# Performance work log

Measured on AMD Instinct MI355X. Metric: run time of the kernel, lower is better.

## Reference

```python
import jax, jax.numpy as jnp
import numpy as np

N, E, F_IN, HID, HEADS, B, CLASSES = 50000, 800000, 128, 64, 4, 512, 2


def setup_inputs() -> dict:
    key = jax.random.key(0)
    ks = jax.random.split(key, 20)
    s = 0.05
    inp = {
        "x": jax.random.normal(ks[0], (N, F_IN), jnp.float32),
        "edge_index": jax.random.randint(ks[1], (2, E), 0, N, jnp.int32),
        "batch": jnp.sort(jax.random.randint(ks[2], (N,), 0, B, jnp.int32)),
        # GCN layers (3): layer0 F_IN->HID, layers 1,2 HID->HID
        "gcn_w0": jax.random.normal(ks[3], (F_IN, HID), jnp.float32) * s,
        "gcn_b0": jnp.zeros((HID,), jnp.float32),
        "gcn_w1": jax.random.normal(ks[4], (HID, HID), jnp.float32) * s,
        "gcn_b1": jnp.zeros((HID,), jnp.float32),
        "gcn_w2": jax.random.normal(ks[5], (HID, HID), jnp.float32) * s,
        "gcn_b2": jnp.zeros((HID,), jnp.float32),
        # GAT: W [HID, HEADS*HID], attention vectors [HEADS, HID], bias [HID] (concat=False)
        "gat_w": jax.random.normal(ks[6], (HID, HEADS * HID), jnp.float32) * s,
        "gat_att_src": jax.random.normal(ks[7], (HEADS, HID), jnp.float32) * s,
        "gat_att_dst": jax.random.normal(ks[8], (HEADS, HID), jnp.float32) * s,
        "gat_b": jnp.zeros((HID,), jnp.float32),
        # MLP head
        "lin1_w": jax.random.normal(ks[9], (HID, HID // 2), jnp.float32) * s,
        "lin1_b": jnp.zeros((HID // 2,), jnp.float32),
        "lin2_w": jax.random.normal(ks[10], (HID // 2, CLASSES), jnp.float32) * s,
        "lin2_b": jnp.zeros((CLASSES,), jnp.float32),
    }
    return inp


def _forward(x, edge_index, batch,
             gcn_w0, gcn_b0, gcn_w1, gcn_b1, gcn_w2, gcn_b2,
             gat_w, gat_att_src, gat_att_dst, gat_b,
             lin1_w, lin1_b, lin2_w, lin2_b):
    n = x.shape[0]
    loop = jnp.arange(n, dtype=edge_index.dtype)
    src = jnp.concatenate([edge_index[0], loop])  # [E+N] with self-loops
    dst = jnp.concatenate([edge_index[1], loop])

    # symmetric GCN normalization (self-loops included, deg >= 1)
    deg = jax.ops.segment_sum(jnp.ones_like(dst, dtype=x.dtype), dst, num_segments=n)
    dinv = jax.lax.rsqrt(jnp.maximum(deg, 1.0))
    norm = dinv[src] * dinv[dst]  # [E+N]

    for W, b in ((gcn_w0, gcn_b0), (gcn_w1, gcn_b1), (gcn_w2, gcn_b2)):
        h = x @ W  # [N, HID]
        x = jax.ops.segment_sum(h[src] * norm[:, None], dst, num_segments=n) + b
        x = jax.nn.relu(x)  # dropout is identity in eval mode

    # GAT layer (heads=HEADS, concat=False -> mean over heads)
    H, C = gat_att_src.shape
    h = (x @ gat_w).reshape(n, H, C)  # [N, H, C]
    a_src = jnp.einsum('nhc,hc->nh', h, gat_att_src)
    a_dst = jnp.einsum('nhc,hc->nh', h, gat_att_dst)
    e = jax.nn.leaky_relu(a_src[src] + a_dst[dst], 0.2)  # [E+N, H]
    m = jax.ops.segment_max(e, dst, num_segments=n)      # per-dst softmax max
    p = jnp.exp(e - m[dst])
    denom = jax.ops.segment_sum(p, dst, num_segments=n)
    alpha = p / denom[dst]                                # [E+N, H]
    out = jax.ops.segment_sum(h[src] * alpha[:, :, None], dst, num_segments=n)
    x = jax.nn.relu(out.mean(axis=1) + gat_b)             # [N, HID]

    # global mean pool + global max pool over graphs
    cnt = jax.ops.segment_sum(jnp.ones((n,), x.dtype), batch, num_segments=B)
    mean_p = jax.ops.segment_sum(x, batch, num_segments=B) / jnp.maximum(cnt, 1.0)[:, None]
    max_p = jax.ops.segment_max(x, batch, num_segments=B)
    max_p = jnp.where(cnt[:, None] > 0, max_p, 0.0)
    g = mean_p + max_p  # [B, HID]

    g = jax.nn.relu(g @ lin1_w + lin1_b)
    return g @ lin2_w + lin2_b  # [B, CLASSES]


def reference(x, edge_index, batch,
              gcn_w0, gcn_b0, gcn_w1, gcn_b1, gcn_w2, gcn_b2,
              gat_w, gat_att_src, gat_att_dst, gat_b,
              lin1_w, lin1_b, lin2_w, lin2_b):
    return _forward(x, edge_index, batch,
                    gcn_w0, gcn_b0, gcn_w1, gcn_b1, gcn_w2, gcn_b2,
                    gat_w, gat_att_src, gat_att_dst, gat_b,
                    lin1_w, lin1_b, lin2_w, lin2_b)
```

## Files before the change

### kernel.cpp

```cpp
#include <hip/hip_runtime.h>
#include <math.h>

typedef short bf8 __attribute__((ext_vector_type(8)));
typedef _Float16 h8 __attribute__((ext_vector_type(8)));
typedef float f4 __attribute__((ext_vector_type(4)));
typedef unsigned short ushort_t;

#define BRANGE 128
#define NB_E 256

__device__ __forceinline__ int ilanebcast(int v, int l) {
  return __builtin_amdgcn_readlane(v, l);
}

__device__ __forceinline__ float wave_sum(float v) {
#pragma unroll
  for (int off = 32; off > 0; off >>= 1) v += __shfl_xor(v, off, 64);
  return v;
}

__device__ __forceinline__ ushort_t f2bf(float x) {
  unsigned int u = __float_as_uint(x);
  return (ushort_t)((u + 0x7fffu + ((u >> 16) & 1u)) >> 16);
}
__device__ __forceinline__ float b2f(ushort_t h) {
  return __uint_as_float(((unsigned int)h) << 16);
}

__global__ __launch_bounds__(256) void k_ehist(const int* __restrict__ dst,
                                               int* __restrict__ bhistT, int E, int nbuk) {
  __shared__ int h[512];
  int b = blockIdx.x, tid = threadIdx.x;
  for (int i = tid; i < nbuk; i += 256) h[i] = 0;
  __syncthreads();
  int chunk = (E + gridDim.x - 1) / gridDim.x;
  int e0 = b * chunk, e1 = min(E, e0 + chunk);
  for (int e = e0 + tid; e < e1; e += 256) atomicAdd(&h[dst[e] >> 7], 1);
  __syncthreads();
  for (int i = tid; i < nbuk; i += 256) bhistT[i * NB_E + b] = h[i];
}

__global__ __launch_bounds__(256) void k_btot(const int* __restrict__ bhistT,
                                              int* __restrict__ bcnt, int nb) {
  __shared__ int sm[256];
  int b = blockIdx.x, tid = threadIdx.x;
  sm[tid] = (tid < nb) ? bhistT[b * NB_E + tid] : 0;
  __syncthreads();
  for (int off = 128; off > 0; off >>= 1) {
    if (tid < off) sm[tid] += sm[tid + off];
    __syncthreads();
  }
  if (tid == 0) bcnt[b] = sm[0];
}

__global__ __launch_bounds__(512) void k_bscan(
    const int* __restrict__ bcnt, int* __restrict__ edgebase, int nbuk,
    int* __restrict__ rowstart, int n, int E) {
  __shared__ int smem[512];
  int t = threadIdx.x;
  int v = (t < nbuk) ? bcnt[t] : 0;
  smem[t] = v;
  __syncthreads();
  for (int off = 1; off < 512; off <<= 1) {
    int u = (t >= off) ? smem[t - off] : 0;
    __syncthreads();
    smem[t] += u;
    __syncthreads();
  }
  if (t < nbuk) edgebase[t] = smem[t] - v;
  if (t == 0) rowstart[n] = E + n;
}

__global__ __launch_bounds__(256) void k_bbase(int* __restrict__ bhistT,
                                               const int* __restrict__ edgebase,
                                               int nb) {
  __shared__ int sm[256];
  int b = blockIdx.x, tid = threadIdx.x;
  int v = (tid < nb) ? bhistT[b * NB_E + tid] : 0;
  sm[tid] = v;
  __syncthreads();
  for (int off = 1; off < 256; off <<= 1) {
    int u = (tid >= off) ? sm[tid - off] : 0;
    __syncthreads();
    sm[tid] += u;
    __syncthreads();
  }
  if (tid < nb) bhistT[b * NB_E + tid] = edgebase[b] + sm[tid] - v;
}

__global__ __launch_bounds__(256) void k_ebucket(
    const int* __restrict__ es, const int* __restrict__ ed,
    const int* __restrict__ bhistT, int* __restrict__ bedges, int E, int nbuk) {
  __shared__ int cur[512];
  int b = blockIdx.x, tid = threadIdx.x;
  for (int i = tid; i < nbuk; i += 256) cur[i] = bhistT[i * NB_E + b];
  __syncthreads();
  int chunk = (E + gridDim.x - 1) / gridDim.x;
  int e0 = b * chunk, e1 = min(E, e0 + chunk);
  for (int e = e0 + tid; e < e1; e += 256) {
    int s = es[e], d = ed[e];
    int pos = atomicAdd(&cur[d >> 7], 1);
    bedges[pos] = (s << 7) | (d & 127);
  }
}

__global__ __launch_bounds__(256) void k_ebsort(
    const int* __restrict__ bedges, const int* __restrict__ edgebase,
    const int* __restrict__ bcnt, int* __restrict__ colidx,
    int* __restrict__ rowstart, float* __restrict__ dinv, int n) {
  __shared__ int h[128];
  __shared__ int c[128];
  int b = blockIdx.x, tid = threadIdx.x;
  int nodes0 = b * BRANGE;
  int nnode = min(BRANGE, n - nodes0);
  int ebase = edgebase[b], ecnt = bcnt[b];
  int colbase = ebase + nodes0;
  if (tid < 128) h[tid] = (tid < nnode) ? 1 : 0;
  __syncthreads();
  for (int k = ebase + tid; k < ebase + ecnt; k += 256)
    atomicAdd(&h[bedges[k] & 127], 1);
  __syncthreads();
  int own = (tid < 128) ? h[tid] : 0;
  for (int off = 1; off < 128; off <<= 1) {
    int t = (tid >= off && tid < 128) ? h[tid - off] : 0;
    __syncthreads();
    if (tid < 128) h[tid] += t;
    __syncthreads();
  }
  if (tid < nnode) {
    int excl = h[tid] - own;
    int node = nodes0 + tid;
    rowstart[node] = colbase + excl;
    dinv[node] = 1.0f / sqrtf((float)own);
    colidx[colbase + excl] = node;
    c[tid] = excl + 1;
  }
  __syncthreads();
  for (int k = ebase + tid; k < ebase + ecnt; k += 256) {
    int p = bedges[k];
    int pos = atomicAdd(&c[p & 127], 1);
    colidx[colbase + pos] = p >> 7;
  }
}

__global__ __launch_bounds__(256) void k_wswz_all(
    const float* __restrict__ W0, ushort_t* __restrict__ B0h, ushort_t* __restrict__ B0l,
    const float* __restrict__ W1, _Float16* __restrict__ Bw1h, _Float16* __restrict__ Bw1l,
    const float* __restrict__ W2, _Float16* __restrict__ Bw2h, _Float16* __restrict__ Bw2l,
    const float* __restrict__ Wg, _Float16* __restrict__ Bgh, _Float16* __restrict__ Bgl) {
  int bid = blockIdx.x, tid = threadIdx.x;
  if (bid < 4) {
    int e = bid * 256 + tid;
    int lane = e & 63, kc = (e >> 6) & 3, ct = e >> 8;
    int k0 = kc * 32 + (lane >> 4) * 8;
    int col = ct * 16 + (lane & 15);
#pragma unroll
    for (int j = 0; j < 8; j++) {
      float w = W0[(k0 + j) * 64 + col];
      ushort_t h = f2bf(w);
      B0h[(size_t)e * 8 + j] = h;
      B0l[(size_t)e * 8 + j] = f2bf(w - b2f(h));
    }
  } else if (bid < 8) {
    const float* W = (bid < 6) ? W1 : W2;
    _Float16* Bh = (bid < 6) ? Bw1h : Bw2h;
    _Float16* Bl = (bid < 6) ? Bw1l : Bw2l;
    int e = ((bid - 4) & 1) * 256 + tid;
    int lane = e & 63, kc = (e >> 6) & 1, ct = e >> 7;
    int k0 = kc * 32 + (lane >> 4) * 8;
    int col = ct * 16 + (lane & 15);
#pragma unroll
    for (int j = 0; j < 8; j++) {
      float w = W[(k0 + j) * 64 + col];
      _Float16 h = (_Float16)w;
      Bh[(size_t)e * 8 + j] = h;
      Bl[(size_t)e * 8 + j] = (_Float16)(w - (float)h);
    }
  } else {
    int e = (bid - 8) * 256 + tid;
    int lane = e & 63, kc = (e >> 6) & 7, ct = e >> 9;
    int k0 = kc * 32 + (lane >> 4) * 8;
    int col = ct * 16 + (lane & 15);
#pragma unroll
    for (int j = 0; j < 8; j++) {
      int k = k0 + j;
      float w = Wg[(k & 63) * 256 + (k >> 6) * 64 + col];
      _Float16 h = (_Float16)w;
      Bgh[(size_t)e * 8 + j] = h;
      Bgl[(size_t)e * 8 + j] = (_Float16)(w - (float)h);
    }
  }
}

__global__ __launch_bounds__(256) void k_qprep(
    const float* __restrict__ W, const float* __restrict__ att_s,
    const float* __restrict__ att_d, _Float16* __restrict__ Bq) {
  __shared__ float qs[256], qd[256];
  int t = threadIdx.x;
  int h = t >> 6, k = t & 63;
  float ss = 0.0f, sd = 0.0f;
  for (int c = 0; c < 64; c++) {
    float w = W[k * 256 + h * 64 + c];
    ss = fmaf(w, att_s[h * 64 + c], ss);
    sd = fmaf(w, att_d[h * 64 + c], sd);
  }
  qs[h * 64 + k] = ss;
  qd[h * 64 + k] = sd;
  __syncthreads();
  if (t < 128) {
    int lane = t & 63, kc = t >> 6;
    int k0 = kc * 32 + (lane >> 4) * 8;
    int col = lane & 15;
#pragma unroll
    for (int j = 0; j < 8; j++) {
      int kk = k0 + j;
      float v = (col < 4) ? qs[col * 64 + kk]
                          : ((col < 8) ? qd[(col - 4) * 64 + kk] : 0.0f);
      Bq[(size_t)t * 8 + j] = (_Float16)v;
    }
  }
}

__global__ __launch_bounds__(256) void k_gemm0_mfma(
    const float* __restrict__ X, const ushort_t* __restrict__ Bh,
    const ushort_t* __restrict__ Bl, const float* __restrict__ dinv,
    _Float16* __restrict__ H, int n, int ntiles) {
  int tid = threadIdx.x, lane = tid & 63, wave = tid >> 6;
  int m = lane & 15, q = lane >> 4;
  for (int tile = blockIdx.x * 4 + wave; tile < ntiles; tile += gridDim.x * 4) {
    int ra = tile * 16 + m;
    if (ra >= n) ra = n - 1;
    const float* xrow = X + (size_t)ra * 128;
    f4 acc[4];
#pragma unroll
    for (int ct = 0; ct < 4; ct++) acc[ct] = (f4){0.f, 0.f, 0.f, 0.f};
#pragma unroll 2
    for (int kc = 0; kc < 4; kc++) {
      int ko = kc * 32 + q * 8;
      float4 xa = *(const float4*)(xrow + ko);
      float4 xb = *(const float4*)(xrow + ko + 4);
      float f[8] = {xa.x, xa.y, xa.z, xa.w, xb.x, xb.y, xb.z, xb.w};
      union { ushort_t u[8]; bf8 v; } Uh, Ul;
#pragma unroll
      for (int j = 0; j < 8; j++) {
        ushort_t h = f2bf(f[j]);
        Uh.u[j] = h;
        Ul.u[j] = f2bf(f[j] - b2f(h));
      }
#pragma unroll
      for (int ct = 0; ct < 4; ct++) {
        size_t boff = ((size_t)(ct * 4 + kc) * 64 + lane) * 8;
        bf8 bh = *(const bf8*)(Bh + boff);
        bf8 bl = *(const bf8*)(Bl + boff);
        acc[ct] = __builtin_amdgcn_mfma_f32_16x16x32_bf16(Uh.v, bh, acc[ct], 0, 0, 0);
        acc[ct] = __builtin_amdgcn_mfma_f32_16x16x32_bf16(Ul.v, bh, acc[ct], 0, 0, 0);
        acc[ct] = __builtin_amdgcn_mfma_f32_16x16x32_bf16(Uh.v, bl, acc[ct], 0, 0, 0);
      }
    }
#pragma unroll
    for (int r = 0; r < 4; r++) {
      int row = tile * 16 + q * 4 + r;
      if (row < n) {
        float dv = dinv[row];
#pragma unroll
        for (int ct = 0; ct < 4; ct++)
          H[(size_t)row * 64 + ct * 16 + m] = (_Float16)(acc[ct][r] * dv);
      }
    }
  }
}

__device__ __forceinline__ float gather_sum(const _Float16* __restrict__ h_in,
                                            const int* __restrict__ colidx,
                                            int s0, int s1, int lane) {
  float acc = 0.0f, accB = 0.0f;
  for (int base = s0; base < s1; base += 64) {
    int cnt = min(64, s1 - base);
    int myidx = (lane < cnt) ? colidx[base + lane] : 0;
    int k = 0;
    for (; k + 7 < cnt; k += 8) {
      int i0 = (ilanebcast(myidx, k) << 6) + lane;
      int i1 = (ilanebcast(myidx, k + 1) << 6) + lane;
      int i2 = (ilanebcast(myidx, k + 2) << 6) + lane;
      int i3 = (ilanebcast(myidx, k + 3) << 6) + lane;
      int i4 = (ilanebcast(myidx, k + 4) << 6) + lane;
      int i5 = (ilanebcast(myidx, k + 5) << 6) + lane;
      int i6 = (ilanebcast(myidx, k + 6) << 6) + lane;
      int i7 = (ilanebcast(myidx, k + 7) << 6) + lane;
      float v0 = (float)h_in[i0];
      float v1 = (float)h_in[i1];
      float v2 = (float)h_in[i2];
      float v3 = (float)h_in[i3];
      float v4 = (float)h_in[i4];
      float v5 = (float)h_in[i5];
      float v6 = (float)h_in[i6];
      float v7 = (float)h_in[i7];
      acc += v0; accB += v1; acc += v2; accB += v3;
      acc += v4; accB += v5; acc += v6; accB += v7;
    }
    for (; k + 3 < cnt; k += 4) {
      int i0 = (ilanebcast(myidx, k) << 6) + lane;
      int i1 = (ilanebcast(myidx, k + 1) << 6) + lane;
      int i2 = (ilanebcast(myidx, k + 2) << 6) + lane;
      int i3 = (ilanebcast(myidx, k + 3) << 6) + lane;
      acc += (float)h_in[i0]; accB += (float)h_in[i1];
      acc += (float)h_in[i2]; accB += (float)h_in[i3];
    }
    for (; k < cnt; k++) {
      int i0 = (ilanebcast(myidx, k) << 6) + lane;
      acc += (float)h_in[i0];
    }
  }
  return acc + accB;
}

__global__ __launch_bounds__(1024) void k_agg_gemm_mfma(
    const _Float16* __restrict__ h_in, const float* __restrict__ dinv,
    const int* __restrict__ rowstart, const int* __restrict__ colidx,
    const float* __restrict__ bias, const _Float16* __restrict__ Bh,
    const _Float16* __restrict__ Bl, _Float16* __restrict__ h_out, int n) {
  __shared__ __align__(16) _Float16 xstage[16][72];
  int tid = threadIdx.x, lane = tid & 63, w = tid >> 6;
  int tile = blockIdx.x;
  int node = tile * 16 + w;
  float xv = 0.0f;
  if (node < n) {
    int s0 = rowstart[node], s1 = rowstart[node + 1];
    float a = gather_sum(h_in, colidx, s0, s1, lane);
    xv = fmaxf(fmaf(dinv[node], a, bias[lane]), 0.0f);
  }
  xstage[w][lane] = (_Float16)xv;
  __syncthreads();
  if (w < 4) {
    int m = lane & 15, q = lane >> 4, ct = w;
    h8 af0 = *(const h8*)&xstage[m][q * 8];
    h8 af1 = *(const h8*)&xstage[m][32 + q * 8];
    size_t o0 = ((size_t)(ct * 2 + 0) * 64 + lane) * 8;
    size_t o1 = ((size_t)(ct * 2 + 1) * 64 + lane) * 8;
    h8 bh0 = *(const h8*)(Bh + o0);
    h8 bh1 = *(const h8*)(Bh + o1);
    h8 bl0 = *(const h8*)(Bl + o0);
    h8 bl1 = *(const h8*)(Bl + o1);
    f4 acc = (f4){0.f, 0.f, 0.f, 0.f};
    acc = __builtin_amdgcn_mfma_f32_16x16x32_f16(af0, bh0, acc, 0, 0, 0);
    acc = __builtin_amdgcn_mfma_f32_16x16x32_f16(af1, bh1, acc, 0, 0, 0);
    acc = __builtin_amdgcn_mfma_f32_16x16x32_f16(af0, bl0, acc, 0, 0, 0);
    acc = __builtin_amdgcn_mfma_f32_16x16x32_f16(af1, bl1, acc, 0, 0, 0);
#pragma unroll
    for (int r = 0; r < 4; r++) {
      int n2 = tile * 16 + q * 4 + r;
      if (n2 < n)
        h_out[(size_t)n2 * 64 + ct * 16 + m] = (_Float16)(acc[r] * dinv[n2]);
    }
  }
}

__global__ __launch_bounds__(1024) void k_agg_gatpre_mfma(
    const _Float16* __restrict__ h_in, const float* __restrict__ dinv,
    const int* __restrict__ rowstart, const int* __restrict__ colidx,
    const float* __restrict__ bias, const _Float16* __restrict__ Bq,
    _Float16* __restrict__ x3, float* __restrict__ a_src, float* __restrict__ a_dst,
    int n) {
  __shared__ __align__(16) _Float16 xstage[16][72];
  int tid = threadIdx.x, lane = tid & 63, w = tid >> 6;
  int tile = blockIdx.x;
  int node = tile * 16 + w;
  float xv = 0.0f;
  if (node < n) {
    int s0 = rowstart[node], s1 = rowstart[node + 1];
    float a = gather_sum(h_in, colidx, s0, s1, lane);
    xv = fmaxf(fmaf(dinv[node], a, bias[lane]), 0.0f);
    x3[(node << 6) + lane] = (_Float16)xv;
  }
  xstage[w][lane] = (_Float16)xv;
  __syncthreads();
  if (w == 0) {
    int m = lane & 15, q = lane >> 4;
    h8 af0 = *(const h8*)&xstage[m][q * 8];
    h8 af1 = *(const h8*)&xstage[m][32 + q * 8];
    h8 bq0 = *(const h8*)(Bq + (size_t)lane * 8);
    h8 bq1 = *(const h8*)(Bq + (size_t)(64 + lane) * 8);
    f4 accL = (f4){0.f, 0.f, 0.f, 0.f};
    accL = __builtin_amdgcn_mfma_f32_16x16x32_f16(af0, bq0, accL, 0, 0, 0);
    accL = __builtin_amdgcn_mfma_f32_16x16x32_f16(af1, bq1, accL, 0, 0, 0);
#pragma unroll
    for (int r = 0; r < 4; r++) {
      int n2 = tile * 16 + q * 4 + r;
      if (n2 < n) {
        if (m < 4) a_src[(size_t)n2 * 4 + m] = accL[r];
        else if (m < 8) a_dst[(size_t)n2 * 4 + (m - 4)] = accL[r];
      }
    }
  }
}

__global__ __launch_bounds__(1024) void k_gat_fused(
    const _Float16* __restrict__ x3, const float* __restrict__ a_src,
    const float* __restrict__ a_dst, const int* __restrict__ rowstart,
    const int* __restrict__ colidx, const _Float16* __restrict__ Bh,
    const _Float16* __restrict__ Bl, const float* __restrict__ bias,
    float* __restrict__ out, int n) {
  __shared__ __align__(16) float4 wlds[16][64];
  __shared__ float astage[16][261];
  int tid = threadIdx.x, lane = tid & 63, w = tid >> 6;
  int tile = blockIdx.x;
  int node = tile * 16 + w;
  float v0 = 0.f, v1 = 0.f, v2 = 0.f, v3 = 0.f;
  if (node < n) {
    const float4 adv = *(const float4*)&a_dst[(size_t)node * 4];
    int s0 = rowstart[node], s1 = rowstart[node + 1];
    float acc0 = 0, acc1 = 0, acc2 = 0, acc3 = 0;
    float S0 = 0, S1 = 0, S2 = 0, S3 = 0;
    for (int base = s0; base < s1; base += 64) {
      int cnt = min(64, s1 - base);
      bool act = (lane < cnt);
      int myidx = act ? colidx[base + lane] : 0;
      float w0 = 0, w1 = 0, w2 = 0, w3 = 0;
      if (act) {
        const float4 as = *(const float4*)&a_src[(size_t)myidx * 4];
        float e0 = as.x + adv.x; e0 = (e0 > 0.f) ? e0 : 0.2f * e0; w0 = __expf(e0);
        float e1 = as.y + adv.y; e1 = (e1 > 0.f) ? e1 : 0.2f * e1; w1 = __expf(e1);
        float e2 = as.z + adv.z; e2 = (e2 > 0.f) ? e2 : 0.2f * e2; w2 = __expf(e2);
        float e3 = as.w + adv.w; e3 = (e3 > 0.f) ? e3 : 0.2f * e3; w3 = __expf(e3);
      }
      S0 += wave_sum(w0); S1 += wave_sum(w1);
      S2 += wave_sum(w2); S3 += wave_sum(w3);
      wlds[w][lane] = make_float4(w0, w1, w2, w3);
      int k = 0;
      for (; k + 3 < cnt; k += 4) {
        int i0 = (ilanebcast(myidx, k) << 6) + lane;
        int i1 = (ilanebcast(myidx, k + 1) << 6) + lane;
        int i2 = (ilanebcast(myidx, k + 2) << 6) + lane;
        int i3 = (ilanebcast(myidx, k + 3) << 6) + lane;
        float4 wa = wlds[w][k];
        float4 wb = wlds[w][k + 1];
        float4 wc = wlds[w][k + 2];
        float4 wd = wlds[w][k + 3];
        float va = (float)x3[i0];
        float vb = (float)x3[i1];
        float vc = (float)x3[i2];
        float vd = (float)x3[i3];
        acc0 = fmaf(wa.x, va, acc0); acc1 = fmaf(wa.y, va, acc1);
        acc2 = fmaf(wa.z, va, acc2); acc3 = fmaf(wa.w, va, acc3);
        acc0 = fmaf(wb.x, vb, acc0); acc1 = fmaf(wb.y, vb, acc1);
        acc2 = fmaf(wb.z, vb, acc2); acc3 = fmaf(wb.w, vb, acc3);
        acc0 = fmaf(wc.x, vc, acc0); acc1 = fmaf(wc.y, vc, acc1);
        acc2 = fmaf(wc.z, vc, acc2); acc3 = fmaf(wc.w, vc, acc3);
        acc0 = fmaf(wd.x, vd, acc0); acc1 = fmaf(wd.y, vd, acc1);
        acc2 = fmaf(wd.z, vd, acc2); acc3 = fmaf(wd.w, vd, acc3);
      }
      for (; k < cnt; k++) {
        int i0 = (ilanebcast(myidx, k) << 6) + lane;
        float4 wa = wlds[w][k];
        float va = (float)x3[i0];
        acc0 = fmaf(wa.x, va, acc0); acc1 = fmaf(wa.y, va, acc1);
        acc2 = fmaf(wa.z, va, acc2); acc3 = fmaf(wa.w, va, acc3);
      }
    }
    v0 = acc0 * (0.25f / S0);
    v1 = acc1 * (0.25f / S1);
    v2 = acc2 * (0.25f / S2);
    v3 = acc3 * (0.25f / S3);
  }
  astage[w][lane] = v0;
  astage[w][64 + lane] = v1;
  astage[w][128 + lane] = v2;
  astage[w][192 + lane] = v3;
  __syncthreads();
  if (w < 4) {
    int m = lane & 15, q = lane >> 4, ct = w;
    float bv = bias[ct * 16 + m];
    f4 acc = (f4){0.f, 0.f, 0.f, 0.f};
#pragma unroll 2
    for (int kc = 0; kc < 8; kc++) {
      const float* ap = &astage[m][kc * 32 + q * 8];
      union { _Float16 u[8]; h8 v; } Uh, Ul;
#pragma unroll
      for (int j = 0; j < 8; j++) {
        float a = ap[j];
        _Float16 h = (_Float16)a;
        Uh.u[j] = h;
        Ul.u[j] = (_Float16)(a - (float)h);
      }
      size_t boff = ((size_t)(ct * 8 + kc) * 64 + lane) * 8;
      h8 bh = *(const h8*)(Bh + boff);
      h8 bl = *(const h8*)(Bl + boff);
      acc = __builtin_amdgcn_mfma_f32_16x16x32_f16(Uh.v, bh, acc, 0, 0, 0);
      acc = __builtin_amdgcn_mfma_f32_16x16x32_f16(Ul.v, bh, acc, 0, 0, 0);
      acc = __builtin_amdgcn_mfma_f32_16x16x32_f16(Uh.v, bl, acc, 0, 0, 0);
    }
#pragma unroll
    for (int r = 0; r < 4; r++) {
      int row = tile * 16 + q * 4 + r;
      if (row < n)
        out[(size_t)row * 64 + ct * 16 + m] = fmaxf(acc[r] + bv, 0.f);
    }
  }
}

__global__ __launch_bounds__(256) void k_pool_mlp(
    const float* __restrict__ x, const int* __restrict__ batch,
    const float* __restrict__ w1, const float* __restrict__ b1,
    const float* __restrict__ w2, const float* __restrict__ b2,
    float* __restrict__ out, int n, int B) {
  __shared__ float gls[4][64];
  int tid = threadIdx.x, lane = tid & 63, w = tid >> 6;
  int g = blockIdx.x * 4 + w;
  if (g >= B) return;
  int lo = 0, hi = n;
  while (lo < hi) { int mid = (lo + hi) >> 1; if (batch[mid] < g) lo = mid + 1; else hi = mid; }
  int s0 = lo;
  lo = 0; hi = n;
  while (lo < hi) { int mid = (lo + hi) >> 1; if (batch[mid] < g + 1) lo = mid + 1; else hi = mid; }
  int s1 = lo;
  float sum = 0.0f, mx = -INFINITY;
  for (int nd = s0; nd < s1; ++nd) {
    float v = x[(size_t)nd * 64 + lane];
    sum += v;
    mx = fmaxf(mx, v);
  }
  int cnt = s1 - s0;
  float mean = sum / fmaxf((float)cnt, 1.0f);
  float mp = (cnt > 0) ? mx : 0.0f;
  gls[w][lane] = mean + mp;
  float a = 0.0f;
  if (lane < 32) {
    a = b1[lane];
    for (int i = 0; i < 64; i++) a = fmaf(gls[w][i], w1[i * 32 + lane], a);
    a = fmaxf(a, 0.0f);
  }
  float p0 = (lane < 32) ? a * w2[lane * 2 + 0] : 0.0f;
  float p1 = (lane < 32) ? a * w2[lane * 2 + 1] : 0.0f;
  p0 = wave_sum(p0);
  p1 = wave_sum(p1);
  if (lane == 0) {
    out[g * 2 + 0] = b2[0] + p0;
    out[g * 2 + 1] = b2[1] + p1;
  }
}

extern "C" void kernel_launch(void* const* d_in, const int* in_sizes, int n_in,
                              void* d_out, int out_size, void* d_ws, size_t ws_size,
                              hipStream_t stream) {
  const float* x     = (const float*)d_in[0];
  const int*   ei    = (const int*)d_in[1];
  const int*   batch = (const int*)d_in[2];
  const float* w0 = (const float*)d_in[3];  const float* b0 = (const float*)d_in[4];
  const float* w1 = (const float*)d_in[5];  const float* b1 = (const float*)d_in[6];
  const float* w2 = (const float*)d_in[7];  const float* b2 = (const float*)d_in[8];
  const float* gat_w = (const float*)d_in[9];
  const float* att_s = (const float*)d_in[10];
  const float* att_d = (const float*)d_in[11];
  const float* gat_b = (const float*)d_in[12];
  const float* l1w = (const float*)d_in[13]; const float* l1b = (const float*)d_in[14];
  const float* l2w = (const float*)d_in[15]; const float* l2b = (const float*)d_in[16];

  const int N = in_sizes[0] / 128;
  const int E = in_sizes[1] / 2;
  const int B = out_size / 2;
  const int NT = (N + 15) / 16;
  const int NBUK = (N + BRANGE - 1) / BRANGE;

  char* ws = (char*)d_ws;
  size_t off = 0;
  auto alloc = [&](size_t bytes) -> void* {
    void* p = ws + off;
    off = (off + bytes + 255) & ~(size_t)255;
    return p;
  };
  int*       bhistT   = (int*)alloc((size_t)NBUK * NB_E * 4);
  int*       edgebase = (int*)alloc((size_t)NBUK * 4);
  int*       bcnt     = (int*)alloc((size_t)NBUK * 4);
  int*       bedges   = (int*)alloc((size_t)E * 4);
  int*       rowstart = (int*)alloc((size_t)(N + 1) * 4);
  int*       colidx   = (int*)alloc((size_t)(E + N) * 4);
  float*     dinv     = (float*)alloc((size_t)N * 4);
  _Float16*  hbuf     = (_Float16*)alloc((size_t)N * 64 * 2);
  _Float16*  hbuf2    = (_Float16*)alloc((size_t)N * 64 * 2);
  _Float16*  xg       = (_Float16*)alloc((size_t)N * 64 * 2);
  float*     gatout   = (float*)alloc((size_t)N * 64 * 4);
  float*     a_src    = (float*)alloc((size_t)N * 4 * 4);
  float*     a_dst    = (float*)alloc((size_t)N * 4 * 4);
  ushort_t*  B0h      = (ushort_t*)alloc(4 * 4 * 64 * 8 * 2);
  ushort_t*  B0l      = (ushort_t*)alloc(4 * 4 * 64 * 8 * 2);
  _Float16*  Bw1h     = (_Float16*)alloc(8 * 64 * 8 * 2);
  _Float16*  Bw1l     = (_Float16*)alloc(8 * 64 * 8 * 2);
  _Float16*  Bw2h     = (_Float16*)alloc(8 * 64 * 8 * 2);
  _Float16*  Bw2l     = (_Float16*)alloc(8 * 64 * 8 * 2);
  _Float16*  Bq       = (_Float16*)alloc(2 * 64 * 8 * 2);
  _Float16*  Bgh      = (_Float16*)alloc(4 * 8 * 64 * 8 * 2);
  _Float16*  Bgl      = (_Float16*)alloc(4 * 8 * 64 * 8 * 2);
  (void)ws_size; (void)n_in;

  k_ehist<<<NB_E, 256, 0, stream>>>(ei + E, bhistT, E, NBUK);
  k_btot<<<NBUK, 256, 0, stream>>>(bhistT, bcnt, NB_E);
  k_bscan<<<1, 512, 0, stream>>>(bcnt, edgebase, NBUK, rowstart, N, E);
  k_bbase<<<NBUK, 256, 0, stream>>>(bhistT, edgebase, NB_E);
  k_ebucket<<<NB_E, 256, 0, stream>>>(ei, ei + E, bhistT, bedges, E, NBUK);
  k_ebsort<<<NBUK, 256, 0, stream>>>(bedges, edgebase, bcnt, colidx, rowstart, dinv, N);
  k_qprep<<<1, 256, 0, stream>>>(gat_w, att_s, att_d, Bq);
  k_wswz_all<<<16, 256, 0, stream>>>(w0, B0h, B0l, w1, Bw1h, Bw1l,
                                     w2, Bw2h, Bw2l, gat_w, Bgh, Bgl);

  k_gemm0_mfma<<<1024, 256, 0, stream>>>(x, B0h, B0l, dinv, hbuf, N, NT);
  k_agg_gemm_mfma<<<NT, 1024, 0, stream>>>(hbuf, dinv, rowstart, colidx, b0,
                                           Bw1h, Bw1l, hbuf2, N);
  k_agg_gemm_mfma<<<NT, 1024, 0, stream>>>(hbuf2, dinv, rowstart, colidx, b1,
                                           Bw2h, Bw2l, hbuf, N);
  k_agg_gatpre_mfma<<<NT, 1024, 0, stream>>>(hbuf, dinv, rowstart, colidx, b2,
                                             Bq, xg, a_src, a_dst, N);
  k_gat_fused<<<NT, 1024, 0, stream>>>(xg, a_src, a_dst, rowstart, colidx,
                                       Bgh, Bgl, gat_b, gatout, N);
  k_pool_mlp<<<(B + 3) / 4, 256, 0, stream>>>(gatout, batch, l1w, l1b, l2w, l2b,
                                              (float*)d_out, N, B);
}
```

Baseline: 342.3 us.

## Sort nodes by degree so aggregation blocks process nodes of similar degree

Adds a counting sort of nodes by in-degree: a per-block degree histogram, then total, scan and base passes that reuse the bucket kernels, then a scatter that builds a permutation. The three GCN aggregation kernels and the fused GAT kernel now take their 16 nodes per block from this permutation, and write outputs through the permuted node ids kept in shared memory. The aim is to cut load imbalance inside each 1024-thread block, where every wave waits at the barrier for the slowest-degree node before the MFMA step. In exchange it costs five extra small launches and makes the output row writes scattered rather than contiguous.

```diff
diff --git a/kernel.cpp b/kernel.cpp
--- a/kernel.cpp
+++ b/kernel.cpp
@@ -140,6 +140,38 @@
     int p = bedges[k];
     int pos = atomicAdd(&c[p & 127], 1);
     colidx[colbase + pos] = p >> 7;
+  }
+}
+
+__global__ __launch_bounds__(256) void k_dhist(const int* __restrict__ rowstart,
+                                               int* __restrict__ dhistT, int n) {
+  __shared__ int h[256];
+  int b = blockIdx.x, tid = threadIdx.x;
+  h[tid] = 0;
+  __syncthreads();
+  int chunk = (n + gridDim.x - 1) / gridDim.x;
+  int i0 = b * chunk, i1 = min(n, i0 + chunk);
+  for (int i = i0 + tid; i < i1; i += 256) {
+    int deg = min(rowstart[i + 1] - rowstart[i], 255);
+    atomicAdd(&h[deg], 1);
+  }
+  __syncthreads();
+  dhistT[tid * NB_E + b] = h[tid];
+}
+
+__global__ __launch_bounds__(256) void k_dscatter(const int* __restrict__ rowstart,
+                                                  const int* __restrict__ dhistT,
+                                                  int* __restrict__ perm, int n) {
+  __shared__ int cur[256];
+  int b = blockIdx.x, tid = threadIdx.x;
+  cur[tid] = dhistT[tid * NB_E + b];
+  __syncthreads();
+  int chunk = (n + gridDim.x - 1) / gridDim.x;
+  int i0 = b * chunk, i1 = min(n, i0 + chunk);
+  for (int i = i0 + tid; i < i1; i += 256) {
+    int deg = min(rowstart[i + 1] - rowstart[i], 255);
+    int pos = atomicAdd(&cur[deg], 1);
+    perm[pos] = i;
   }
 }
 
@@ -317,14 +349,18 @@
 __global__ __launch_bounds__(1024) void k_agg_gemm_mfma(
     const _Float16* __restrict__ h_in, const float* __restrict__ dinv,
     const int* __restrict__ rowstart, const int* __restrict__ colidx,
+    const int* __restrict__ perm,
     const float* __restrict__ bias, const _Float16* __restrict__ Bh,
     const _Float16* __restrict__ Bl, _Float16* __restrict__ h_out, int n) {
   __shared__ __align__(16) _Float16 xstage[16][72];
+  __shared__ int pnode[16];
   int tid = threadIdx.x, lane = tid & 63, w = tid >> 6;
   int tile = blockIdx.x;
-  int node = tile * 16 + w;
+  int idx = tile * 16 + w;
+  int node = (idx < n) ? perm[idx] : -1;
+  if (lane == 0) pnode[w] = node;
   float xv = 0.0f;
-  if (node < n) {
+  if (node >= 0) {
     int s0 = rowstart[node], s1 = rowstart[node + 1];
     float a = gather_sum(h_in, colidx, s0, s1, lane);
     xv = fmaxf(fmaf(dinv[node], a, bias[lane]), 0.0f);
@@ -348,8 +384,8 @@
     acc = __builtin_amdgcn_mfma_f32_16x16x32_f16(af1, bl1, acc, 0, 0, 0);
 #pragma unroll
     for (int r = 0; r < 4; r++) {
-      int n2 = tile * 16 + q * 4 + r;
-      if (n2 < n)
+      int n2 = pnode[q * 4 + r];
+      if (n2 >= 0)
         h_out[(size_t)n2 * 64 + ct * 16 + m] = (_Float16)(acc[r] * dinv[n2]);
     }
   }
@@ -358,15 +394,19 @@
 __global__ __launch_bounds__(1024) void k_agg_gatpre_mfma(
     const _Float16* __restrict__ h_in, const float* __restrict__ dinv,
     const int* __restrict__ rowstart, const int* __restrict__ colidx,
+    const int* __restrict__ perm,
     const float* __restrict__ bias, const _Float16* __restrict__ Bq,
     _Float16* __restrict__ x3, float* __restrict__ a_src, float* __restrict__ a_dst,
     int n) {
   __shared__ __align__(16) _Float16 xstage[16][72];
+  __shared__ int pnode[16];
   int tid = threadIdx.x, lane = tid & 63, w = tid >> 6;
   int tile = blockIdx.x;
-  int node = tile * 16 + w;
+  int idx = tile * 16 + w;
+  int node = (idx < n) ? perm[idx] : -1;
+  if (lane == 0) pnode[w] = node;
   float xv = 0.0f;
-  if (node < n) {
+  if (node >= 0) {
     int s0 = rowstart[node], s1 = rowstart[node + 1];
     float a = gather_sum(h_in, colidx, s0, s1, lane);
     xv = fmaxf(fmaf(dinv[node], a, bias[lane]), 0.0f);
@@ -385,8 +425,8 @@
     accL = __builtin_amdgcn_mfma_f32_16x16x32_f16(af1, bq1, accL, 0, 0, 0);
 #pragma unroll
     for (int r = 0; r < 4; r++) {
-      int n2 = tile * 16 + q * 4 + r;
-      if (n2 < n) {
+      int n2 = pnode[q * 4 + r];
+      if (n2 >= 0) {
         if (m < 4) a_src[(size_t)n2 * 4 + m] = accL[r];
         else if (m < 8) a_dst[(size_t)n2 * 4 + (m - 4)] = accL[r];
       }
@@ -397,16 +437,20 @@
 __global__ __launch_bounds__(1024) void k_gat_fused(
     const _Float16* __restrict__ x3, const float* __restrict__ a_src,
     const float* __restrict__ a_dst, const int* __restrict__ rowstart,
-    const int* __restrict__ colidx, const _Float16* __restrict__ Bh,
+    const int* __restrict__ colidx, const int* __restrict__ perm,
+    const _Float16* __restrict__ Bh,
     const _Float16* __restrict__ Bl, const float* __restrict__ bias,
     float* __restrict__ out, int n) {
   __shared__ __align__(16) float4 wlds[16][64];
   __shared__ float astage[16][261];
+  __shared__ int pnode[16];
   int tid = threadIdx.x, lane = tid & 63, w = tid >> 6;
   int tile = blockIdx.x;
-  int node = tile * 16 + w;
+  int idx = tile * 16 + w;
+  int node = (idx < n) ? perm[idx] : -1;
+  if (lane == 0) pnode[w] = node;
   float v0 = 0.f, v1 = 0.f, v2 = 0.f, v3 = 0.f;
-  if (node < n) {
+  if (node >= 0) {
     const float4 adv = *(const float4*)&a_dst[(size_t)node * 4];
     int s0 = rowstart[node], s1 = rowstart[node + 1];
     float acc0 = 0, acc1 = 0, acc2 = 0, acc3 = 0;
@@ -491,8 +535,8 @@
     }
 #pragma unroll
     for (int r = 0; r < 4; r++) {
-      int row = tile * 16 + q * 4 + r;
-      if (row < n)
+      int row = pnode[q * 4 + r];
+      if (row >= 0)
         out[(size_t)row * 64 + ct * 16 + m] = fmaxf(acc[r] + bv, 0.f);
     }
   }
@@ -575,6 +619,10 @@
   int*       rowstart = (int*)alloc((size_t)(N + 1) * 4);
   int*       colidx   = (int*)alloc((size_t)(E + N) * 4);
   float*     dinv     = (float*)alloc((size_t)N * 4);
+  int*       dhistT   = (int*)alloc((size_t)256 * NB_E * 4);
+  int*       dcnt     = (int*)alloc(256 * 4);
+  int*       dbase    = (int*)alloc(256 * 4);
+  int*       perm     = (int*)alloc((size_t)N * 4);
   _Float16*  hbuf     = (_Float16*)alloc((size_t)N * 64 * 2);
   _Float16*  hbuf2    = (_Float16*)alloc((size_t)N * 64 * 2);
   _Float16*  xg       = (_Float16*)alloc((size_t)N * 64 * 2);
@@ -598,18 +646,23 @@
   k_bbase<<<NBUK, 256, 0, stream>>>(bhistT, edgebase, NB_E);
   k_ebucket<<<NB_E, 256, 0, stream>>>(ei, ei + E, bhistT, bedges, E, NBUK);
   k_ebsort<<<NBUK, 256, 0, stream>>>(bedges, edgebase, bcnt, colidx, rowstart, dinv, N);
+  k_dhist<<<NB_E, 256, 0, stream>>>(rowstart, dhistT, N);
+  k_btot<<<256, 256, 0, stream>>>(dhistT, dcnt, NB_E);
+  k_bscan<<<1, 512, 0, stream>>>(dcnt, dbase, 256, rowstart, N, E);
+  k_bbase<<<256, 256, 0, stream>>>(dhistT, dbase, NB_E);
+  k_dscatter<<<NB_E, 256, 0, stream>>>(rowstart, dhistT, perm, N);
   k_qprep<<<1, 256, 0, stream>>>(gat_w, att_s, att_d, Bq);
   k_wswz_all<<<16, 256, 0, stream>>>(w0, B0h, B0l, w1, Bw1h, Bw1l,
                                      w2, Bw2h, Bw2l, gat_w, Bgh, Bgl);
 
   k_gemm0_mfma<<<1024, 256, 0, stream>>>(x, B0h, B0l, dinv, hbuf, N, NT);
-  k_agg_gemm_mfma<<<NT, 1024, 0, stream>>>(hbuf, dinv, rowstart, colidx, b0,
+  k_agg_gemm_mfma<<<NT, 1024, 0, stream>>>(hbuf, dinv, rowstart, colidx, perm, b0,
                                            Bw1h, Bw1l, hbuf2, N);
-  k_agg_gemm_mfma<<<NT, 1024, 0, stream>>>(hbuf2, dinv, rowstart, colidx, b1,
+  k_agg_gemm_mfma<<<NT, 1024, 0, stream>>>(hbuf2, dinv, rowstart, colidx, perm, b1,
                                            Bw2h, Bw2l, hbuf, N);
-  k_agg_gatpre_mfma<<<NT, 1024, 0, stream>>>(hbuf, dinv, rowstart, colidx, b2,
+  k_agg_gatpre_mfma<<<NT, 1024, 0, stream>>>(hbuf, dinv, rowstart, colidx, perm, b2,
                                              Bq, xg, a_src, a_dst, N);
-  k_gat_fused<<<NT, 1024, 0, stream>>>(xg, a_src, a_dst, rowstart, colidx,
+  k_gat_fused<<<NT, 1024, 0, stream>>>(xg, a_src, a_dst, rowstart, colidx, perm,
                                        Bgh, Bgl, gat_b, gatout, N);
   k_pool_mlp<<<(B + 3) / 4, 256, 0, stream>>>(gatout, batch, l1w, l1b, l2w, l2b,
                                               (float*)d_out, N, B);
```

After: 365.2 us. +6.7%, slower.
